# Performance work log

Hardware: AMD Instinct MI355X
Metric: run time of the kernel (lower is better)

Reference implementation:

```python
import jax, jax.numpy as jnp
import numpy as np

N = 50000   # nodes
D = 128     # hidden_dim == in_dim
H = 4       # heads
C = 32      # hidden_dim // heads
L = 3       # message_layers
ET = 640000 # temporal edges
EH = 320000 # host edges


def layer_norm(x, g, b, eps=1e-5):
    m = x.mean(-1, keepdims=True)
    v = ((x - m) ** 2).mean(-1, keepdims=True)
    return (x - m) / jnp.sqrt(v + eps) * g + b


def transformer_conv(h, src, dst, e_emb, Wq, bq, Wk, bk, Wv, bv, We, Ws, bs):
    # PyG TransformerConv, concat=True, root_weight=True, beta=False
    n = h.shape[0]
    q = (h @ Wq + bq).reshape(n, H, C)
    k = (h @ Wk + bk).reshape(n, H, C)
    v = (h @ Wv + bv).reshape(n, H, C)
    ee = (e_emb @ We).reshape(-1, H, C)          # lin_edge has no bias
    kj = k[src] + ee                              # [E,H,C]
    a = (q[dst] * kj).sum(-1) / np.sqrt(C)        # [E,H]
    amax = jax.ops.segment_max(a, dst, num_segments=n)
    amax = jnp.where(jnp.isfinite(amax), amax, 0.0)
    ex = jnp.exp(a - amax[dst])
    den = jax.ops.segment_sum(ex, dst, num_segments=n)
    alpha = ex / (den[dst] + 1e-16)               # segment softmax over in-edges of dst
    msg = (v[src] + ee) * alpha[..., None]        # [E,H,C]
    out = jax.ops.segment_sum(msg, dst, num_segments=n).reshape(n, H * C)
    return out + h @ Ws + bs                      # root/skip connection


def mlp_head(h, W1, b1, g, bt, W2, b2):
    z = jax.nn.silu(h @ W1 + b1)
    z = layer_norm(z, g, bt)
    return z @ W2 + b2


def setup_inputs() -> dict:
    key = jax.random.key(0)
    ks = iter(jax.random.split(key, 80))
    nrm = lambda shape: jax.random.normal(next(ks), shape, jnp.float32) * 0.05
    inp = {}
    inp['x'] = jax.random.normal(next(ks), (N, D), jnp.float32)
    inp['edge_index_temporal'] = jax.random.randint(next(ks), (2, ET), 0, N)
    inp['edge_index_host'] = jax.random.randint(next(ks), (2, EH), 0, N)
    inp['edge_attr_temporal'] = jax.random.uniform(next(ks), (ET, 1), jnp.float32)
    inp['edge_attr_host'] = jax.random.normal(next(ks), (EH, 3), jnp.float32)
    # edge encoders
    inp['W_tedge'] = nrm((1, 4)); inp['b_tedge'] = jnp.zeros(4)
    inp['W_hedge'] = nrm((3, 4)); inp['b_hedge'] = jnp.zeros(4)
    # stacked conv params [L, ...] for temporal (_t) and host (_h) convs
    for s in ('t', 'h'):
        inp[f'Wq_{s}'] = nrm((L, D, D)); inp[f'bq_{s}'] = jnp.zeros((L, D))
        inp[f'Wk_{s}'] = nrm((L, D, D)); inp[f'bk_{s}'] = jnp.zeros((L, D))
        inp[f'Wv_{s}'] = nrm((L, D, D)); inp[f'bv_{s}'] = jnp.zeros((L, D))
        inp[f'We_{s}'] = nrm((L, 4, D))
        inp[f'Ws_{s}'] = nrm((L, D, D)); inp[f'bs_{s}'] = jnp.zeros((L, D))
    inp['norm_g'] = jnp.ones((L, D)); inp['norm_b'] = jnp.zeros((L, D))
    inp['fg'] = jnp.ones(D); inp['fb'] = jnp.zeros(D)
    inp['dW1'] = nrm((D, D)); inp['db1'] = jnp.zeros(D)
    inp['dg'] = jnp.ones(D); inp['dbt'] = jnp.zeros(D)
    inp['dW2'] = nrm((D, 3)); inp['db2'] = jnp.zeros(3)
    inp['sW1'] = nrm((D, D)); inp['sb1'] = jnp.zeros(D)
    inp['sg'] = jnp.ones(D); inp['sbt'] = jnp.zeros(D)
    inp['sW2'] = nrm((D, 3)); inp['sb2'] = jnp.zeros(3)
    return inp


def reference(x, edge_index_temporal, edge_index_host, edge_attr_temporal, edge_attr_host,
              W_tedge, b_tedge, W_hedge, b_hedge,
              Wq_t, bq_t, Wk_t, bk_t, Wv_t, bv_t, We_t, Ws_t, bs_t,
              Wq_h, bq_h, Wk_h, bk_h, Wv_h, bv_h, We_h, Ws_h, bs_h,
              norm_g, norm_b, fg, fb,
              dW1, db1, dg, dbt, dW2, db2,
              sW1, sb1, sg, sbt, sW2, sb2):
    te = edge_attr_temporal @ W_tedge + b_tedge   # [ET, edge_dim]
    he = edge_attr_host @ W_hedge + b_hedge       # [EH, edge_dim]
    st, dt_ = edge_index_temporal[0], edge_index_temporal[1]
    sh, dh = edge_index_host[0], edge_index_host[1]
    h = x
    for l in range(L):
        t_out = transformer_conv(h, st, dt_, te, Wq_t[l], bq_t[l], Wk_t[l], bk_t[l],
                                 Wv_t[l], bv_t[l], We_t[l], Ws_t[l], bs_t[l])
        h_out = transformer_conv(h, sh, dh, he, Wq_h[l], bq_h[l], Wk_h[l], bk_h[l],
                                 Wv_h[l], bv_h[l], We_h[l], Ws_h[l], bs_h[l])
        combined = jax.nn.silu(layer_norm(t_out + h_out, norm_g[l], norm_b[l]))
        h = h + combined  # residual (shapes match since in_dim == hidden_dim)
    h = layer_norm(h, fg, fb)
    drift = mlp_head(h, dW1, db1, dg, dbt, dW2, db2)
    diff = mlp_head(h, sW1, sb1, sg, sbt, sW2, sb2)
    return drift, diff
```

## Files before the change

### kernel.cpp

```cpp
#include <hip/hip_runtime.h>
#include <math.h>

#define NN 50000
#define DD 128
#define ET_N 640000
#define EH_N 320000
#define NL 3

static inline int cdiv(int a, int b){ return (a+b-1)/b; }

typedef __attribute__((ext_vector_type(8))) short short8;
typedef __attribute__((ext_vector_type(4))) float f32x4;

__device__ float   g_h [(size_t)NN*DD];
__device__ unsigned short g_hb[(size_t)NN*DD];
__device__ unsigned short g_Wb[(size_t)NL*8*DD*DD];
__device__ float   g_Q [2][(size_t)NN*DD];
__device__ float   g_S [2][(size_t)NN*DD];
__device__ ushort2 g_KV[2][(size_t)NN*DD];
__device__ float   g_to[(size_t)NN*DD];
__device__ float   g_ho[(size_t)NN*DD];
__device__ int     g_cnt[2][NN];
__device__ int     g_cur[2][NN];
__device__ int     g_rs [2][NN+1];
__device__ int     g_srcc[2][ET_N];
__device__ float   g_ta[ET_N];
__device__ float4  g_ha[EH_N];

__device__ inline unsigned short f2bf(float f){
  unsigned u = __float_as_uint(f);
  unsigned r = (u + 0x7fffu + ((u>>16)&1u)) >> 16;
  return (unsigned short)r;
}
__device__ inline float bf2f(unsigned short s){
  return __uint_as_float(((unsigned)s)<<16);
}

__global__ void k_copy_h(const float* __restrict__ x){
  int i = blockIdx.x*256 + threadIdx.x;
  if (i < NN*DD/4){
    float4 v = reinterpret_cast<const float4*>(x)[i];
    reinterpret_cast<float4*>(g_h)[i] = v;
    ushort4 b; b.x=f2bf(v.x); b.y=f2bf(v.y); b.z=f2bf(v.z); b.w=f2bf(v.w);
    reinterpret_cast<ushort4*>(g_hb)[i] = b;
  }
}

__global__ void k_zero_cnt(){
  int i = blockIdx.x*256 + threadIdx.x;
  if (i < NN) g_cnt[blockIdx.y][i] = 0;
}

struct WPtrs { const float* W[24]; };
__global__ __launch_bounds__(256) void k_cvtw(WPtrs wp){
  int mat = blockIdx.y;
  const float* W = wp.W[mat];
  int e = blockIdx.x*256 + threadIdx.x;
  int n = e >> 7, k = e & 127;
  g_Wb[(size_t)mat*DD*DD + e] = f2bf(W[k*DD+n]);
}

__global__ void k_hist(const int* __restrict__ dstT, const int* __restrict__ dstH){
  int which = blockIdx.y;
  int E = which ? EH_N : ET_N;
  const int* dst = which ? dstH : dstT;
  int e = blockIdx.x*256+threadIdx.x;
  if (e<E) atomicAdd(&g_cnt[which][dst[e]], 1);
}

__global__ __launch_bounds__(1024) void k_scan(){
  int which = blockIdx.y;
  int* row_start = g_rs[which];
  const int* cnt = g_cnt[which];
  int* cur = g_cur[which];
  __shared__ int buf[1024];
  int tid = threadIdx.x;
  const int n = NN;
  int chunk = (n + 1023) >> 10;
  int start = tid*chunk; if (start>n) start=n;
  int end = start+chunk; if (end>n) end=n;
  int lsum=0;
  for (int i=start;i<end;++i) lsum += cnt[i];
  buf[tid]=lsum;
  __syncthreads();
  for (int off=1; off<1024; off<<=1){
    int t = (tid>=off)? buf[tid-off]:0;
    __syncthreads();
    buf[tid] += t;
    __syncthreads();
  }
  int run = buf[tid]-lsum;
  for (int i=start;i<end;++i){ row_start[i]=run; cur[i]=run; run += cnt[i]; }
  if (tid==1023) row_start[n]=run;
}

__global__ void k_scatter(const int* __restrict__ eit, const int* __restrict__ eih,
                          const float* __restrict__ attrT, const float* __restrict__ attrH){
  int which = blockIdx.y;
  int e = blockIdx.x*256+threadIdx.x;
  if (which==0){
    if (e>=ET_N) return;
    int src = eit[e], dst = eit[ET_N+e];
    int p = atomicAdd(&g_cur[0][dst],1);
    g_srcc[0][p]=src;
    g_ta[p]=attrT[e];
  } else {
    if (e>=EH_N) return;
    int src = eih[e], dst = eih[EH_N+e];
    int p = atomicAdd(&g_cur[1][dst],1);
    g_srcc[1][p]=src;
    g_ha[p]=make_float4(attrH[e*3+0],attrH[e*3+1],attrH[e*3+2],0.f);
  }
}

struct BiasP { const float* b[8]; };

__global__ __launch_bounds__(256) void k_gemm_mfma(int l, BiasP bp){
  __shared__ unsigned short lA[64*DD];
  __shared__ unsigned short lB[DD*DD];
  int conv = blockIdx.y;
  int setbase = l*8 + conv*4;
  int tid = threadIdx.x;
  int m0 = blockIdx.x*64;

#pragma unroll
  for (int p=0;p<4;++p){
    int c = tid + p*256;
    int row = c >> 4, col16 = c & 15;
    int grow = m0 + row;
    uint4 v = make_uint4(0,0,0,0);
    if (grow < NN) v = *reinterpret_cast<const uint4*>(&g_hb[(size_t)grow*DD + col16*8]);
    int off = (row*256 + col16*16) ^ ((row&7)<<4);
    *reinterpret_cast<uint4*>((char*)lA + off) = v;
  }

  int wave = tid >> 6, lane = tid & 63;
  int lrow = lane & 15, kg = lane >> 4;
  int n0w = wave*32;

  auto stageB = [&](const unsigned short* Wm){
#pragma unroll
    for (int p=0;p<8;++p){
      int c = tid + p*256;
      int row = c >> 4, col16 = c & 15;
      uint4 v = *reinterpret_cast<const uint4*>(&Wm[(size_t)row*DD + col16*8]);
      int off = (row*256 + col16*16) ^ ((row&7)<<4);
      *reinterpret_cast<uint4*>((char*)lB + off) = v;
    }
  };

  stageB(&g_Wb[(size_t)(setbase+0)*DD*DD]);
  __syncthreads();

  short8 a[4][4];
#pragma unroll
  for (int kk=0;kk<4;++kk){
    int kbyte = kk*64 + kg*16;
#pragma unroll
    for (int mi=0;mi<4;++mi){
      int row = mi*16 + lrow;
      int off = (row*256 + kbyte) ^ ((row&7)<<4);
      a[kk][mi] = *reinterpret_cast<const short8*>((char*)lA + off);
    }
  }

  auto computeC = [&](f32x4 (&acc)[4][2]){
#pragma unroll
    for (int mi=0;mi<4;++mi)
#pragma unroll
      for (int ni=0;ni<2;++ni) acc[mi][ni] = (f32x4){0.f,0.f,0.f,0.f};
#pragma unroll
    for (int kk=0;kk<4;++kk){
      int kbyte = kk*64 + kg*16;
      short8 b[2];
#pragma unroll
      for (int ni=0;ni<2;++ni){
        int n = n0w + ni*16 + lrow;
        int off = (n*256 + kbyte) ^ ((n&7)<<4);
        b[ni] = *reinterpret_cast<const short8*>((char*)lB + off);
      }
#pragma unroll
      for (int mi=0;mi<4;++mi)
#pragma unroll
        for (int ni=0;ni<2;++ni)
          acc[mi][ni] = __builtin_amdgcn_mfma_f32_16x16x32_bf16(a[kk][mi], b[ni], acc[mi][ni], 0,0,0);
    }
  };

  f32x4 acc[4][2], accK[4][2];

  computeC(acc);
  {
    const float* bias = bp.b[conv*4+0];
    float* op = g_Q[conv];
#pragma unroll
    for (int ni=0;ni<2;++ni){
      int col = n0w + ni*16 + lrow;
      float bs = bias[col];
#pragma unroll
      for (int mi=0;mi<4;++mi)
#pragma unroll
        for (int r=0;r<4;++r){
          int row = m0 + mi*16 + kg*4 + r;
          if (row < NN) op[(size_t)row*DD + col] = acc[mi][ni][r] + bs;
        }
    }
  }
  __syncthreads();
  stageB(&g_Wb[(size_t)(setbase+1)*DD*DD]);
  __syncthreads();
  computeC(accK);
  __syncthreads();
  stageB(&g_Wb[(size_t)(setbase+2)*DD*DD]);
  __syncthreads();
  computeC(acc);
  {
    const float* bK = bp.b[conv*4+1];
    const float* bV = bp.b[conv*4+2];
#pragma unroll
    for (int ni=0;ni<2;++ni){
      int col = n0w + ni*16 + lrow;
      float bk = bK[col], bv = bV[col];
#pragma unroll
      for (int mi=0;mi<4;++mi)
#pragma unroll
        for (int r=0;r<4;++r){
          int row = m0 + mi*16 + kg*4 + r;
          if (row < NN){
            ushort2 kv;
            kv.x = f2bf(accK[mi][ni][r] + bk);
            kv.y = f2bf(acc [mi][ni][r] + bv);
            g_KV[conv][(size_t)row*DD + col] = kv;
          }
        }
    }
  }
  __syncthreads();
  stageB(&g_Wb[(size_t)(setbase+3)*DD*DD]);
  __syncthreads();
  computeC(acc);
  {
    const float* bias = bp.b[conv*4+3];
    float* op = g_S[conv];
#pragma unroll
    for (int ni=0;ni<2;++ni){
      int col = n0w + ni*16 + lrow;
      float bs = bias[col];
#pragma unroll
      for (int mi=0;mi<4;++mi)
#pragma unroll
        for (int r=0;r<4;++r){
          int row = m0 + mi*16 + kg*4 + r;
          if (row < NN) op[(size_t)row*DD + col] = acc[mi][ni][r] + bs;
        }
    }
  }
}

__device__ inline float waveRed(float v){
  v += __shfl_xor(v,32); v += __shfl_xor(v,16); v += __shfl_xor(v,8);
  v += __shfl_xor(v,4);  v += __shfl_xor(v,2);  v += __shfl_xor(v,1);
  return v;
}
__device__ inline float headRed(float v){
  v += __shfl_xor(v,16); v += __shfl_xor(v,8); v += __shfl_xor(v,4);
  v += __shfl_xor(v,2);  v += __shfl_xor(v,1);
  return v;
}

__global__ __launch_bounds__(128) void k_agg(
    const float* __restrict__ WeT, const float* __restrict__ WeH,
    const float* __restrict__ Wt,  const float* __restrict__ bt4,
    const float* __restrict__ Wh,  const float* __restrict__ bh4){
  int conv = blockIdx.y;
  int i = blockIdx.x;
  int d = threadIdx.x;

  float c0=0.f,c1=0.f,c2=0.f,c3=0.f;
  if (conv==0){
#pragma unroll
    for (int j=0;j<4;++j){ float w=WeT[j*DD+d]; c1 += Wt[j]*w; c0 += bt4[j]*w; }
  } else {
#pragma unroll
    for (int j=0;j<4;++j){
      float w=WeH[j*DD+d];
      c0 += Wh[j]*w; c1 += Wh[4+j]*w; c2 += Wh[8+j]*w; c3 += bh4[j]*w;
    }
  }

  float qd = g_Q[conv][(size_t)i*DD+d];
  float qe0,qe1,qe2=0.f,qe3=0.f;
  if (conv==0){
    qe0 = headRed(qd*c0);
    qe1 = headRed(qd*c1);
  } else {
    qe0 = headRed(qd*c0);
    qe1 = headRed(qd*c1);
    qe2 = headRed(qd*c2);
    qe3 = headRed(qd*c3);
  }

  const int*     srcc = g_srcc[conv];
  const ushort2* KV   = g_KV[conv];
  int beg=g_rs[conv][i], end=g_rs[conv][i+1];
  int cnt = end-beg;

  const float inv32 = 0.17677669529663687f;
  float mA=-INFINITY,dnA=0.f,acA=0.f,x0A=0.f,x1A=0.f,x2A=0.f;
  float mB=-INFINITY,dnB=0.f,acB=0.f,x0B=0.f,x1B=0.f,x2B=0.f;

  if (cnt>0){
    ushort2 kv0=make_ushort2(0,0), kv1=make_ushort2(0,0);
    float4 a0v=make_float4(0.f,0.f,0.f,0.f), a1v=a0v;
    bool h1;
    {
      int s0=srcc[beg];
      if (conv==0) a0v.x=g_ta[beg]; else a0v=g_ha[beg];
      kv0=KV[(size_t)s0*DD+d];
      h1 = (beg+1<end);
      if (h1){
        int s1=srcc[beg+1];
        if (conv==0) a1v.x=g_ta[beg+1]; else a1v=g_ha[beg+1];
        kv1=KV[(size_t)s1*DD+d];
      }
    }
    for (int t=beg; t<end; t+=2){
      ushort2 ckv0=kv0, ckv1=kv1; float4 ca0=a0v, ca1=a1v; bool ch1=h1;
      int tn=t+2;
      if (tn<end){
        int s0=srcc[tn];
        if (conv==0) a0v.x=g_ta[tn]; else a0v=g_ha[tn];
        kv0=KV[(size_t)s0*DD+d];
        h1 = (tn+1<end);
        if (h1){
          int s1=srcc[tn+1];
          if (conv==0) a1v.x=g_ta[tn+1]; else a1v=g_ha[tn+1];
          kv1=KV[(size_t)s1*DD+d];
        }
      }
      float p0 = qd*bf2f(ckv0.x);
      float p1 = ch1 ? qd*bf2f(ckv1.x) : 0.f;
#pragma unroll
      for (int mk=16; mk>=1; mk>>=1){ p0 += __shfl_xor(p0,mk); p1 += __shfl_xor(p1,mk); }
      float lg0, lg1;
      if (conv==0){
        lg0 = (p0 + qe0 + ca0.x*qe1)*inv32;
        lg1 = (p1 + qe0 + ca1.x*qe1)*inv32;
      } else {
        lg0 = (p0 + ca0.x*qe0 + ca0.y*qe1 + ca0.z*qe2 + qe3)*inv32;
        lg1 = (p1 + ca1.x*qe0 + ca1.y*qe1 + ca1.z*qe2 + qe3)*inv32;
      }
      {
        float nm=fmaxf(mA,lg0), sc=__expf(mA-nm), ea=__expf(lg0-nm);
        dnA=dnA*sc+ea; acA=acA*sc+ea*bf2f(ckv0.y);
        x0A=x0A*sc+ea*ca0.x;
        if (conv==1){ x1A=x1A*sc+ea*ca0.y; x2A=x2A*sc+ea*ca0.z; }
        mA=nm;
      }
      if (ch1){
        float nm=fmaxf(mB,lg1), sc=__expf(mB-nm), ea=__expf(lg1-nm);
        dnB=dnB*sc+ea; acB=acB*sc+ea*bf2f(ckv1.y);
        x0B=x0B*sc+ea*ca1.x;
        if (conv==1){ x1B=x1B*sc+ea*ca1.y; x2B=x2B*sc+ea*ca1.z; }
        mB=nm;
      }
    }
  }

  float r;
  if (cnt==0){
    r = 0.f;
  } else {
    float mm = fmaxf(mA,mB);
    float eA = __expf(mA-mm), eB = __expf(mB-mm);
    float den = dnA*eA + dnB*eB;
    float ac  = acA*eA + acB*eB;
    float x0  = x0A*eA + x0B*eB;
    float id = 1.f/den;
    if (conv==0){
      r = ac*id + c0 + c1*(x0*id);
    } else {
      float x1 = x1A*eA + x1B*eB;
      float x2 = x2A*eA + x2B*eB;
      r = ac*id + c0*(x0*id) + c1*(x1*id) + c2*(x2*id) + c3;
    }
  }
  r += g_S[conv][(size_t)i*DD+d];
  float* o = conv ? g_ho : g_to;
  o[(size_t)i*DD+d] = r;
}

__global__ __launch_bounds__(256) void k_combine(const float* __restrict__ g, const float* __restrict__ bt){
  int lane = threadIdx.x & 63;
  int node = blockIdx.x*4 + (threadIdx.x>>6);
  if (node>=NN) return;
  size_t i0 = (size_t)node*DD + lane, i1 = i0+64;
  float v0 = g_to[i0] + g_ho[i0];
  float v1 = g_to[i1] + g_ho[i1];
  float s = waveRed(v0+v1);
  float mean = s*(1.f/128.f);
  float d0=v0-mean, d1=v1-mean;
  float q = waveRed(d0*d0+d1*d1);
  float inv = 1.f/sqrtf(q*(1.f/128.f)+1e-5f);
  float c0 = d0*inv*g[lane]+bt[lane];
  float c1 = d1*inv*g[lane+64]+bt[lane+64];
  float h0 = g_h[i0] + c0/(1.f+__expf(-c0));
  float h1 = g_h[i1] + c1/(1.f+__expf(-c1));
  g_h[i0] = h0; g_h[i1] = h1;
  g_hb[i0] = f2bf(h0); g_hb[i1] = f2bf(h1);
}

__global__ __launch_bounds__(256) void k_finalln(const float* __restrict__ g, const float* __restrict__ b){
  int lane = threadIdx.x & 63;
  int node = blockIdx.x*4 + (threadIdx.x>>6);
  if (node>=NN) return;
  size_t i0 = (size_t)node*DD + lane, i1 = i0+64;
  float v0 = g_h[i0], v1 = g_h[i1];
  float s = waveRed(v0+v1);
  float mean = s*(1.f/128.f);
  float d0=v0-mean, d1=v1-mean;
  float q = waveRed(d0*d0+d1*d1);
  float inv = 1.f/sqrtf(q*(1.f/128.f)+1e-5f);
  g_h[i0]=d0*inv*g[lane]+b[lane];
  g_h[i1]=d1*inv*g[lane+64]+b[lane+64];
}

__global__ __launch_bounds__(128) void k_head(
      const float* __restrict__ W1, const float* __restrict__ b1,
      const float* __restrict__ g, const float* __restrict__ bt,
      const float* __restrict__ W2, const float* __restrict__ b2,
      float* __restrict__ out){
  int d = threadIdx.x;
  int wv = d >> 6;
  int i0 = blockIdx.x*8;
  const int n = NN;
  __shared__ float rows[8][DD];
  __shared__ float comb[2];
#pragma unroll
  for (int t=0;t<8;++t){
    int node = i0+t;
    rows[t][d] = (node<n)? g_h[(size_t)node*DD+d] : 0.f;
  }
  __syncthreads();
  float z[8];
  float b1d = b1[d];
#pragma unroll
  for (int t=0;t<8;++t) z[t]=b1d;
  for (int k=0;k<DD;++k){
    float w = W1[k*DD+d];
#pragma unroll
    for (int t=0;t<8;++t) z[t] += rows[t][k]*w;
  }
#pragma unroll
  for (int t=0;t<8;++t){ float v=z[t]; z[t] = v/(1.f+expf(-v)); }
  float gd=g[d], btd=bt[d];
  float w2a=W2[d*3+0], w2b=W2[d*3+1], w2c=W2[d*3+2];
  float b2a=b2[0], b2b=b2[1], b2c=b2[2];
  for (int t=0;t<8;++t){
    int node=i0+t;
    float zz=z[t];
    float s = waveRed(zz);
    if ((d&63)==0) comb[wv]=s;
    __syncthreads();
    float mean=(comb[0]+comb[1])*(1.f/128.f);
    __syncthreads();
    float dv=zz-mean;
    float q2 = waveRed(dv*dv);
    if ((d&63)==0) comb[wv]=q2;
    __syncthreads();
    float inv = 1.f/sqrtf((comb[0]+comb[1])*(1.f/128.f)+1e-5f);
    __syncthreads();
    float zn = dv*inv*gd+btd;
    float p0 = waveRed(zn*w2a);
    if ((d&63)==0) comb[wv]=p0;
    __syncthreads();
    float o0 = comb[0]+comb[1]+b2a;
    __syncthreads();
    float p1 = waveRed(zn*w2b);
    if ((d&63)==0) comb[wv]=p1;
    __syncthreads();
    float o1 = comb[0]+comb[1]+b2b;
    __syncthreads();
    float p2 = waveRed(zn*w2c);
    if ((d&63)==0) comb[wv]=p2;
    __syncthreads();
    float o2 = comb[0]+comb[1]+b2c;
    __syncthreads();
    if (d==0 && node<n){
      out[(size_t)node*3+0]=o0; out[(size_t)node*3+1]=o1; out[(size_t)node*3+2]=o2;
    }
  }
}

extern "C" void kernel_launch(void* const* d_in, const int* in_sizes, int n_in,
                              void* d_out, int out_size, void* d_ws, size_t ws_size,
                              hipStream_t stream){
  (void)in_sizes; (void)n_in; (void)out_size; (void)d_ws; (void)ws_size;
  const float* x    = (const float*)d_in[0];
  const int*   eit  = (const int*)d_in[1];
  const int*   eih  = (const int*)d_in[2];
  const float* eat  = (const float*)d_in[3];
  const float* eah  = (const float*)d_in[4];
  const float* W_te = (const float*)d_in[5];
  const float* b_te = (const float*)d_in[6];
  const float* W_he = (const float*)d_in[7];
  const float* b_he = (const float*)d_in[8];
  const float *Wq_t=(const float*)d_in[9],  *bq_t=(const float*)d_in[10];
  const float *Wk_t=(const float*)d_in[11], *bk_t=(const float*)d_in[12];
  const float *Wv_t=(const float*)d_in[13], *bv_t=(const float*)d_in[14];
  const float *We_t=(const float*)d_in[15];
  const float *Ws_t=(const float*)d_in[16], *bs_t=(const float*)d_in[17];
  const float *Wq_h=(const float*)d_in[18], *bq_h=(const float*)d_in[19];
  const float *Wk_h=(const float*)d_in[20], *bk_h=(const float*)d_in[21];
  const float *Wv_h=(const float*)d_in[22], *bv_h=(const float*)d_in[23];
  const float *We_h=(const float*)d_in[24];
  const float *Ws_h=(const float*)d_in[25], *bs_h=(const float*)d_in[26];
  const float *norm_g=(const float*)d_in[27], *norm_b=(const float*)d_in[28];
  const float *fg=(const float*)d_in[29], *fb=(const float*)d_in[30];
  const float *dW1=(const float*)d_in[31], *db1=(const float*)d_in[32];
  const float *dg=(const float*)d_in[33],  *dbt=(const float*)d_in[34];
  const float *dW2=(const float*)d_in[35], *db2=(const float*)d_in[36];
  const float *sW1=(const float*)d_in[37], *sb1=(const float*)d_in[38];
  const float *sg=(const float*)d_in[39],  *sbt=(const float*)d_in[40];
  const float *sW2=(const float*)d_in[41], *sb2=(const float*)d_in[42];
  float* outp = (float*)d_out;

  k_copy_h<<<cdiv(NN*DD/4,256),256,0,stream>>>(x);

  WPtrs wp;
  for (int l=0;l<NL;++l){
    wp.W[l*8+0]=Wq_t+(size_t)l*DD*DD; wp.W[l*8+1]=Wk_t+(size_t)l*DD*DD;
    wp.W[l*8+2]=Wv_t+(size_t)l*DD*DD; wp.W[l*8+3]=Ws_t+(size_t)l*DD*DD;
    wp.W[l*8+4]=Wq_h+(size_t)l*DD*DD; wp.W[l*8+5]=Wk_h+(size_t)l*DD*DD;
    wp.W[l*8+6]=Wv_h+(size_t)l*DD*DD; wp.W[l*8+7]=Ws_h+(size_t)l*DD*DD;
  }
  k_cvtw<<<dim3(64,24),256,0,stream>>>(wp);

  k_zero_cnt<<<dim3(cdiv(NN,256),2),256,0,stream>>>();
  k_hist<<<dim3(cdiv(ET_N,256),2),256,0,stream>>>(eit+ET_N, eih+EH_N);
  k_scan<<<dim3(1,2),1024,0,stream>>>();
  k_scatter<<<dim3(cdiv(ET_N,256),2),256,0,stream>>>(eit, eih, eat, eah);

  for (int l=0;l<NL;++l){
    BiasP bp;
    bp.b[0]=bq_t+(size_t)l*DD; bp.b[1]=bk_t+(size_t)l*DD;
    bp.b[2]=bv_t+(size_t)l*DD; bp.b[3]=bs_t+(size_t)l*DD;
    bp.b[4]=bq_h+(size_t)l*DD; bp.b[5]=bk_h+(size_t)l*DD;
    bp.b[6]=bv_h+(size_t)l*DD; bp.b[7]=bs_h+(size_t)l*DD;
    k_gemm_mfma<<<dim3(cdiv(NN,64),2),256,0,stream>>>(l, bp);
    k_agg<<<dim3(NN,2),128,0,stream>>>(We_t+(size_t)l*4*DD, We_h+(size_t)l*4*DD,
                                       W_te, b_te, W_he, b_he);
    k_combine<<<cdiv(NN,4),256,0,stream>>>(norm_g+(size_t)l*DD, norm_b+(size_t)l*DD);
  }
  k_finalln<<<cdiv(NN,4),256,0,stream>>>(fg, fb);
  k_head<<<cdiv(NN,8),128,0,stream>>>(dW1, db1, dg, dbt, dW2, db2, outp);
  k_head<<<cdiv(NN,8),128,0,stream>>>(sW1, sb1, sg, sbt, sW2, sb2, outp+(size_t)NN*3);
}
```

Before: 1.318 ms.

## Aggregate one node per wave with two channels per lane

The edge-aggregation kernel now maps one node to a 64-lane wave, with each lane handling two adjacent channels. Previously a 128-thread block served each node with one channel per thread. Key/value pairs are loaded as 8-byte vectors and the per-head dot-product reduction needs only four shuffle steps instead of five. The two-edge interleaved online softmax is replaced by a single-stream loop with one-edge prefetch. The intent is to halve the thread count and shuffle work per edge and to widen memory accesses, at the cost of less instruction-level parallelism per edge, since only one edge is in flight per wave.

After: 1.224 ms. 7.1% less time.

```diff
diff --git a/kernel.cpp b/kernel.cpp
--- a/kernel.cpp
+++ b/kernel.cpp
@@ -35,6 +35,8 @@
 __device__ inline float bf2f(unsigned short s){
   return __uint_as_float(((unsigned)s)<<16);
 }
+__device__ inline float bf_lo(unsigned u){ return __uint_as_float(u<<16); }
+__device__ inline float bf_hi(unsigned u){ return __uint_as_float(u & 0xffff0000u); }
 
 __global__ void k_copy_h(const float* __restrict__ x){
   int i = blockIdx.x*256 + threadIdx.x;
@@ -262,132 +264,110 @@
   v += __shfl_xor(v,4);  v += __shfl_xor(v,2);  v += __shfl_xor(v,1);
   return v;
 }
-__device__ inline float headRed(float v){
-  v += __shfl_xor(v,16); v += __shfl_xor(v,8); v += __shfl_xor(v,4);
-  v += __shfl_xor(v,2);  v += __shfl_xor(v,1);
+__device__ inline float headRed16(float v){
+  v += __shfl_xor(v,8); v += __shfl_xor(v,4);
+  v += __shfl_xor(v,2); v += __shfl_xor(v,1);
   return v;
 }
 
-__global__ __launch_bounds__(128) void k_agg(
+__global__ __launch_bounds__(256) void k_agg(
     const float* __restrict__ WeT, const float* __restrict__ WeH,
     const float* __restrict__ Wt,  const float* __restrict__ bt4,
     const float* __restrict__ Wh,  const float* __restrict__ bh4){
   int conv = blockIdx.y;
-  int i = blockIdx.x;
-  int d = threadIdx.x;
-
-  float c0=0.f,c1=0.f,c2=0.f,c3=0.f;
+  int wave = threadIdx.x >> 6;
+  int lane = threadIdx.x & 63;
+  int i = blockIdx.x*4 + wave;
+  if (i >= NN) return;
+  int d0 = lane*2;
+
+  float c0a=0.f,c1a=0.f,c2a=0.f,c3a=0.f;
+  float c0b=0.f,c1b=0.f,c2b=0.f,c3b=0.f;
   if (conv==0){
 #pragma unroll
-    for (int j=0;j<4;++j){ float w=WeT[j*DD+d]; c1 += Wt[j]*w; c0 += bt4[j]*w; }
+    for (int j=0;j<4;++j){
+      float wa=WeT[j*DD+d0], wb=WeT[j*DD+d0+1];
+      c1a += Wt[j]*wa; c0a += bt4[j]*wa;
+      c1b += Wt[j]*wb; c0b += bt4[j]*wb;
+    }
   } else {
 #pragma unroll
     for (int j=0;j<4;++j){
-      float w=WeH[j*DD+d];
-      c0 += Wh[j]*w; c1 += Wh[4+j]*w; c2 += Wh[8+j]*w; c3 += bh4[j]*w;
-    }
-  }
-
-  float qd = g_Q[conv][(size_t)i*DD+d];
-  float qe0,qe1,qe2=0.f,qe3=0.f;
-  if (conv==0){
-    qe0 = headRed(qd*c0);
-    qe1 = headRed(qd*c1);
-  } else {
-    qe0 = headRed(qd*c0);
-    qe1 = headRed(qd*c1);
-    qe2 = headRed(qd*c2);
-    qe3 = headRed(qd*c3);
-  }
-
-  const int*     srcc = g_srcc[conv];
-  const ushort2* KV   = g_KV[conv];
+      float wa=WeH[j*DD+d0], wb=WeH[j*DD+d0+1];
+      c0a += Wh[j]*wa; c1a += Wh[4+j]*wa; c2a += Wh[8+j]*wa; c3a += bh4[j]*wa;
+      c0b += Wh[j]*wb; c1b += Wh[4+j]*wb; c2b += Wh[8+j]*wb; c3b += bh4[j]*wb;
+    }
+  }
+
+  float2 q2 = *reinterpret_cast<const float2*>(&g_Q[conv][(size_t)i*DD+d0]);
+  float q0 = q2.x, q1 = q2.y;
+  float qe0 = headRed16(q0*c0a + q1*c0b);
+  float qe1 = headRed16(q0*c1a + q1*c1b);
+  float qe2=0.f, qe3=0.f;
+  if (conv==1){
+    qe2 = headRed16(q0*c2a + q1*c2b);
+    qe3 = headRed16(q0*c3a + q1*c3b);
+  }
+
+  const int*  srcc = g_srcc[conv];
+  const uint2* KV  = reinterpret_cast<const uint2*>(g_KV[conv]);
   int beg=g_rs[conv][i], end=g_rs[conv][i+1];
   int cnt = end-beg;
 
   const float inv32 = 0.17677669529663687f;
-  float mA=-INFINITY,dnA=0.f,acA=0.f,x0A=0.f,x1A=0.f,x2A=0.f;
-  float mB=-INFINITY,dnB=0.f,acB=0.f,x0B=0.f,x1B=0.f,x2B=0.f;
+  float m=-INFINITY, den=0.f, ac0=0.f, ac1=0.f, x0=0.f, x1=0.f, x2=0.f;
 
   if (cnt>0){
-    ushort2 kv0=make_ushort2(0,0), kv1=make_ushort2(0,0);
-    float4 a0v=make_float4(0.f,0.f,0.f,0.f), a1v=a0v;
-    bool h1;
+    uint2 kv; float4 at=make_float4(0.f,0.f,0.f,0.f);
     {
-      int s0=srcc[beg];
-      if (conv==0) a0v.x=g_ta[beg]; else a0v=g_ha[beg];
-      kv0=KV[(size_t)s0*DD+d];
-      h1 = (beg+1<end);
-      if (h1){
-        int s1=srcc[beg+1];
-        if (conv==0) a1v.x=g_ta[beg+1]; else a1v=g_ha[beg+1];
-        kv1=KV[(size_t)s1*DD+d];
+      int s=srcc[beg];
+      if (conv==0) at.x=g_ta[beg]; else at=g_ha[beg];
+      kv = KV[(size_t)s*(DD/2)+lane];
+    }
+    for (int idx=beg; idx<end; ++idx){
+      uint2 ckv=kv; float4 ca=at;
+      if (idx+1<end){
+        int s=srcc[idx+1];
+        if (conv==0) at.x=g_ta[idx+1]; else at=g_ha[idx+1];
+        kv = KV[(size_t)s*(DD/2)+lane];
       }
-    }
-    for (int t=beg; t<end; t+=2){
-      ushort2 ckv0=kv0, ckv1=kv1; float4 ca0=a0v, ca1=a1v; bool ch1=h1;
-      int tn=t+2;
-      if (tn<end){
-        int s0=srcc[tn];
-        if (conv==0) a0v.x=g_ta[tn]; else a0v=g_ha[tn];
-        kv0=KV[(size_t)s0*DD+d];
-        h1 = (tn+1<end);
-        if (h1){
-          int s1=srcc[tn+1];
-          if (conv==0) a1v.x=g_ta[tn+1]; else a1v=g_ha[tn+1];
-          kv1=KV[(size_t)s1*DD+d];
-        }
-      }
-      float p0 = qd*bf2f(ckv0.x);
-      float p1 = ch1 ? qd*bf2f(ckv1.x) : 0.f;
-#pragma unroll
-      for (int mk=16; mk>=1; mk>>=1){ p0 += __shfl_xor(p0,mk); p1 += __shfl_xor(p1,mk); }
-      float lg0, lg1;
-      if (conv==0){
-        lg0 = (p0 + qe0 + ca0.x*qe1)*inv32;
-        lg1 = (p1 + qe0 + ca1.x*qe1)*inv32;
-      } else {
-        lg0 = (p0 + ca0.x*qe0 + ca0.y*qe1 + ca0.z*qe2 + qe3)*inv32;
-        lg1 = (p1 + ca1.x*qe0 + ca1.y*qe1 + ca1.z*qe2 + qe3)*inv32;
-      }
-      {
-        float nm=fmaxf(mA,lg0), sc=__expf(mA-nm), ea=__expf(lg0-nm);
-        dnA=dnA*sc+ea; acA=acA*sc+ea*bf2f(ckv0.y);
-        x0A=x0A*sc+ea*ca0.x;
-        if (conv==1){ x1A=x1A*sc+ea*ca0.y; x2A=x2A*sc+ea*ca0.z; }
-        mA=nm;
-      }
-      if (ch1){
-        float nm=fmaxf(mB,lg1), sc=__expf(mB-nm), ea=__expf(lg1-nm);
-        dnB=dnB*sc+ea; acB=acB*sc+ea*bf2f(ckv1.y);
-        x0B=x0B*sc+ea*ca1.x;
-        if (conv==1){ x1B=x1B*sc+ea*ca1.y; x2B=x2B*sc+ea*ca1.z; }
-        mB=nm;
-      }
-    }
-  }
-
-  float r;
+      float k0=bf_lo(ckv.x), v0=bf_hi(ckv.x);
+      float k1=bf_lo(ckv.y), v1=bf_hi(ckv.y);
+      float p = q0*k0 + q1*k1;
+      p += __shfl_xor(p,8); p += __shfl_xor(p,4); p += __shfl_xor(p,2); p += __shfl_xor(p,1);
+      float lg = (conv==0) ? (p + qe0 + ca.x*qe1)*inv32
+                           : (p + ca.x*qe0 + ca.y*qe1 + ca.z*qe2 + qe3)*inv32;
+      float nm = fmaxf(m,lg);
+      float sc = __expf(m-nm);
+      float ea = __expf(lg-nm);
+      den = den*sc + ea;
+      ac0 = ac0*sc + ea*v0;
+      ac1 = ac1*sc + ea*v1;
+      x0  = x0*sc + ea*ca.x;
+      if (conv==1){ x1 = x1*sc + ea*ca.y; x2 = x2*sc + ea*ca.z; }
+      m = nm;
+    }
+  }
+
+  float r0, r1;
   if (cnt==0){
-    r = 0.f;
+    r0 = 0.f; r1 = 0.f;
   } else {
-    float mm = fmaxf(mA,mB);
-    float eA = __expf(mA-mm), eB = __expf(mB-mm);
-    float den = dnA*eA + dnB*eB;
-    float ac  = acA*eA + acB*eB;
-    float x0  = x0A*eA + x0B*eB;
     float id = 1.f/den;
     if (conv==0){
-      r = ac*id + c0 + c1*(x0*id);
+      float xm = x0*id;
+      r0 = ac0*id + c0a + c1a*xm;
+      r1 = ac1*id + c0b + c1b*xm;
     } else {
-      float x1 = x1A*eA + x1B*eB;
-      float x2 = x2A*eA + x2B*eB;
-      r = ac*id + c0*(x0*id) + c1*(x1*id) + c2*(x2*id) + c3;
-    }
-  }
-  r += g_S[conv][(size_t)i*DD+d];
+      float xm0=x0*id, xm1=x1*id, xm2=x2*id;
+      r0 = ac0*id + c0a*xm0 + c1a*xm1 + c2a*xm2 + c3a;
+      r1 = ac1*id + c0b*xm0 + c1b*xm1 + c2b*xm2 + c3b;
+    }
+  }
+  float2 s2 = *reinterpret_cast<const float2*>(&g_S[conv][(size_t)i*DD+d0]);
   float* o = conv ? g_ho : g_to;
-  o[(size_t)i*DD+d] = r;
+  float2 out2; out2.x = r0 + s2.x; out2.y = r1 + s2.y;
+  *reinterpret_cast<float2*>(&o[(size_t)i*DD+d0]) = out2;
 }
 
 __global__ __launch_bounds__(256) void k_combine(const float* __restrict__ g, const float* __restrict__ bt){
@@ -548,8 +528,8 @@
     bp.b[4]=bq_h+(size_t)l*DD; bp.b[5]=bk_h+(size_t)l*DD;
     bp.b[6]=bv_h+(size_t)l*DD; bp.b[7]=bs_h+(size_t)l*DD;
     k_gemm_mfma<<<dim3(cdiv(NN,64),2),256,0,stream>>>(l, bp);
-    k_agg<<<dim3(NN,2),128,0,stream>>>(We_t+(size_t)l*4*DD, We_h+(size_t)l*4*DD,
-                                       W_te, b_te, W_he, b_he);
+    k_agg<<<dim3(cdiv(NN,4),2),256,0,stream>>>(We_t+(size_t)l*4*DD, We_h+(size_t)l*4*DD,
+                                               W_te, b_te, W_he, b_he);
     k_combine<<<cdiv(NN,4),256,0,stream>>>(norm_g+(size_t)l*DD, norm_b+(size_t)l*DD);
   }
   k_finalln<<<cdiv(NN,4),256,0,stream>>>(fg, fb);
```
